# Kernel tuning notes

Hardware: AMD Instinct MI355X
Metric: run time of the kernel (lower is better)

Reference implementation:

```python
import jax, jax.numpy as jnp
import numpy as np

X_SCALE, X_ZP = 0.03, -66      # int8 quant params (qmin=-128, qmax=127)
Y_SCALE, Y_ZP = 0.025, 160     # uint8 quant params (qmin=0, qmax=255)
M = K = N = 4096


def setup_inputs() -> dict:
    key = jax.random.key(0)
    kx, ky = jax.random.split(key)
    # x holds int8-range values [-128, 127], y holds uint8-range values [0, 255]
    x = jax.random.randint(kx, (M, K), -128, 128, dtype=jnp.int32)
    y = jax.random.randint(ky, (K, N), 0, 256, dtype=jnp.int32)
    return {"x": x, "y": y}


def reference(x, y):
    # dequantize_per_tensor: (q - zero_point) * scale  (values already in [qmin, qmax])
    xf = (x.astype(jnp.float32) - X_ZP) * X_SCALE   # [M, K]
    yf = (y.astype(jnp.float32) - Y_ZP) * Y_SCALE   # [K, N]
    return jnp.matmul(xf, yf)                       # [M, N]
```

## Files before the change

### kernel.cpp

```cpp
#include <hip/hip_runtime.h>
#include <stdint.h>

#define Mdim 4096
#define Kdim 4096
#define Ndim 4096

typedef __attribute__((ext_vector_type(4))) int v4i;
typedef __attribute__((ext_vector_type(16))) int v16i;

__device__ __forceinline__ void gload_lds16(const void* g, void* l) {
  __builtin_amdgcn_global_load_lds(
      (__attribute__((address_space(1))) void*)(uintptr_t)g,
      (__attribute__((address_space(3))) void*)(uint32_t)(uintptr_t)l,
      16, 0, 0);
}

__global__ __launch_bounds__(256) void pack_fused_kernel(
    const int* __restrict__ x, const int* __restrict__ y,
    char* __restrict__ x8, char* __restrict__ yt, int* __restrict__ rsx,
    int* __restrict__ csy) {
  __shared__ int wt[64 * 17];
  const int t = threadIdx.x;
  if (blockIdx.x < Mdim) {
    const int row = blockIdx.x;
    const int4* src = (const int4*)(x + (size_t)row * Kdim);
    int4* dst = (int4*)(x8 + (size_t)row * Kdim);
    int sum = 0;
    int wd[4];
#pragma unroll
    for (int i = 0; i < 4; ++i) {
      int4 v = src[t * 4 + i];
      sum += v.x + v.y + v.z + v.w;
      wd[i] = (v.x & 0xff) | ((v.y & 0xff) << 8) | ((v.z & 0xff) << 16) |
              (v.w << 24);
    }
    dst[t] = make_int4(wd[0], wd[1], wd[2], wd[3]);
#pragma unroll
    for (int o = 32; o > 0; o >>= 1) sum += __shfl_down(sum, o, 64);
    if ((t & 63) == 0) wt[t >> 6] = sum;
    __syncthreads();
    if (t == 0) rsx[row] = wt[0] + wt[1] + wt[2] + wt[3];
  } else {
    const int bidx = blockIdx.x - Mdim;
    const int n0 = (bidx & 63) * 64;
    const int k0 = (bidx >> 6) * 64;
    const int c = t & 15;
    const int r0 = t >> 4;
#pragma unroll
    for (int s = 0; s < 4; ++s) {
      const int r = r0 + s * 16;
      int4 v = *(const int4*)(y + (size_t)(k0 + r) * Ndim + n0 + c * 4);
      v.x -= 128; v.y -= 128; v.z -= 128; v.w -= 128;
      wt[r * 17 + c] = (v.x & 0xff) | ((v.y & 0xff) << 8) |
                       ((v.z & 0xff) << 16) | (v.w << 24);
    }
    __syncthreads();
    const int n = t >> 2;
    const int kq = t & 3;
    const int colw = n >> 2;
    const int byi = (n & 3) * 8;
    int outw[4];
    int bsum = 0;
#pragma unroll
    for (int j = 0; j < 4; ++j) {
      int b[4];
#pragma unroll
      for (int jj = 0; jj < 4; ++jj) {
        const int word = wt[(kq * 16 + j * 4 + jj) * 17 + colw];
        b[jj] = (word >> byi) & 0xff;
        bsum += (int)(char)b[jj];
      }
      outw[j] = b[0] | (b[1] << 8) | (b[2] << 16) | (b[3] << 24);
    }
    *(int4*)(yt + (size_t)(n0 + n) * Kdim + k0 + kq * 16) =
        make_int4(outw[0], outw[1], outw[2], outw[3]);
    bsum += __shfl_xor(bsum, 1, 64);
    bsum += __shfl_xor(bsum, 2, 64);
    if (kq == 0) atomicAdd(csy + n0 + n, bsum);
  }
}

__global__ __launch_bounds__(512, 2) void gemm_i8_kernel(
    const char* __restrict__ A, const char* __restrict__ B,
    const int* __restrict__ rsx, const int* __restrict__ csy,
    float* __restrict__ out) {
  __shared__ __align__(16) char lds[3 * 32768];
  const int t = threadIdx.x;
  const int l = t & 63;
  const int w = t >> 6;
  const int warow = w >> 1;
  const int wbcol = w & 1;
  const int bm = blockIdx.y * 256;
  const int bn = blockIdx.x * 256;

  v16i acc[2][4];
#pragma unroll
  for (int i = 0; i < 2; ++i)
#pragma unroll
    for (int j = 0; j < 4; ++j)
#pragma unroll
      for (int q = 0; q < 16; ++q) acc[i][j][q] = 0;

  const int srow = t >> 2;
  const int cswz = ((t & 3) ^ ((t >> 3) & 3)) * 16;
  const char* gA = A + (size_t)(bm + srow) * Kdim + cswz;
  const char* gB = B + (size_t)(bn + srow) * Kdim + cswz;

#define STAGE(buf_off, koff)                                                  \
  do {                                                                        \
    _Pragma("unroll") for (int i = 0; i < 2; ++i)                             \
        gload_lds16(gA + (koff) + (size_t)i * 128 * Kdim,                     \
                    lds + (buf_off) + i * 8192 + t * 16);                     \
    _Pragma("unroll") for (int i = 0; i < 2; ++i)                             \
        gload_lds16(gB + (koff) + (size_t)i * 128 * Kdim,                     \
                    lds + (buf_off) + 16384 + i * 8192 + t * 16);             \
  } while (0)

#define STG(sbo, koff, idx)                                                   \
  gload_lds16(((idx) < 2 ? gA : gB) + (koff) + (size_t)((idx)&1) * 128 * Kdim,\
              lds + (sbo) + ((idx) < 2 ? 0 : 16384) + ((idx)&1) * 8192 +      \
                  t * 16)

  const int arow = warow * 64 + (l & 31);
  const int brow = wbcol * 128 + (l & 31);
  const int lhalf = l >> 5;
  const int lkey = (l >> 1) & 3;
  const int slot0 = ((0 + lhalf) ^ lkey) * 16;
  const int slot1 = ((2 + lhalf) ^ lkey) * 16;

#define MFMA(a, b, c) __builtin_amdgcn_mfma_i32_32x32x32_i8(a, b, c, 0, 0, 0)
#define SETP(n) __builtin_amdgcn_s_setprio(n)
#define FENCE() __builtin_amdgcn_sched_barrier(0)
#define BAR()                                                                 \
  do {                                                                        \
    asm volatile("" ::: "memory");                                            \
    __builtin_amdgcn_s_barrier();                                             \
    asm volatile("" ::: "memory");                                            \
  } while (0)
#define WAITV(n) asm volatile("s_waitcnt vmcnt(" #n ")" ::: "memory")

#define TILE(bo, sbo, skoff, dostage, TAILWAIT)                               \
  do {                                                                        \
    const char* As = lds + (bo);                                              \
    const char* Bs = lds + (bo) + 16384;                                      \
    v4i a0, a1, b0, b1;                                                       \
    a0 = *(const v4i*)(As + arow * 64 + slot0);                               \
    a1 = *(const v4i*)(As + (arow + 32) * 64 + slot0);                        \
    b0 = *(const v4i*)(Bs + brow * 64 + slot0);                               \
    b1 = *(const v4i*)(Bs + (brow + 32) * 64 + slot0);                        \
    if (dostage) STG(sbo, skoff, 0);                                          \
    BAR();                                                                    \
    FENCE();                                                                  \
    SETP(1);                                                                  \
    acc[0][0] = MFMA(a0, b0, acc[0][0]);                                      \
    acc[0][1] = MFMA(a0, b1, acc[0][1]);                                      \
    acc[1][0] = MFMA(a1, b0, acc[1][0]);                                      \
    acc[1][1] = MFMA(a1, b1, acc[1][1]);                                      \
    SETP(0);                                                                  \
    FENCE();                                                                  \
    BAR();                                                                    \
    {                                                                         \
      v4i b2 = *(const v4i*)(Bs + (brow + 64) * 64 + slot0);                  \
      v4i b3 = *(const v4i*)(Bs + (brow + 96) * 64 + slot0);                  \
      if (dostage) STG(sbo, skoff, 1);                                        \
      BAR();                                                                  \
      FENCE();                                                                \
      SETP(1);                                                                \
      acc[0][2] = MFMA(a0, b2, acc[0][2]);                                    \
      acc[0][3] = MFMA(a0, b3, acc[0][3]);                                    \
      acc[1][2] = MFMA(a1, b2, acc[1][2]);                                    \
      acc[1][3] = MFMA(a1, b3, acc[1][3]);                                    \
      SETP(0);                                                                \
      FENCE();                                                                \
      BAR();                                                                  \
    }                                                                         \
    a0 = *(const v4i*)(As + arow * 64 + slot1);                               \
    a1 = *(const v4i*)(As + (arow + 32) * 64 + slot1);                        \
    b0 = *(const v4i*)(Bs + brow * 64 + slot1);                               \
    b1 = *(const v4i*)(Bs + (brow + 32) * 64 + slot1);                        \
    if (dostage) STG(sbo, skoff, 2);                                          \
    BAR();                                                                    \
    FENCE();                                                                  \
    SETP(1);                                                                  \
    acc[0][0] = MFMA(a0, b0, acc[0][0]);                                      \
    acc[0][1] = MFMA(a0, b1, acc[0][1]);                                      \
    acc[1][0] = MFMA(a1, b0, acc[1][0]);                                      \
    acc[1][1] = MFMA(a1, b1, acc[1][1]);                                      \
    SETP(0);                                                                  \
    FENCE();                                                                  \
    BAR();                                                                    \
    {                                                                         \
      v4i b2 = *(const v4i*)(Bs + (brow + 64) * 64 + slot1);                  \
      v4i b3 = *(const v4i*)(Bs + (brow + 96) * 64 + slot1);                  \
      if (dostage) STG(sbo, skoff, 3);                                        \
      BAR();                                                                  \
      FENCE();                                                                \
      SETP(1);                                                                \
      acc[0][2] = MFMA(a0, b2, acc[0][2]);                                    \
      acc[0][3] = MFMA(a0, b3, acc[0][3]);                                    \
      acc[1][2] = MFMA(a1, b2, acc[1][2]);                                    \
      acc[1][3] = MFMA(a1, b3, acc[1][3]);                                    \
      SETP(0);                                                                \
      FENCE();                                                                \
      TAILWAIT;                                                               \
      BAR();                                                                  \
    }                                                                         \
  } while (0)

  STAGE(0, 0);
  STAGE(32768, 64);
  WAITV(4);
  BAR();

#pragma unroll 1
  for (int kt = 0; kt < 60; kt += 3) {
    TILE(0, 65536, (kt + 2) * 64, 1, WAITV(4));
    TILE(32768, 0, (kt + 3) * 64, 1, WAITV(4));
    TILE(65536, 32768, (kt + 4) * 64, 1, WAITV(4));
  }
  TILE(0, 65536, 62 * 64, 1, WAITV(4));
  TILE(32768, 0, 63 * 64, 1, WAITV(4));
  TILE(65536, 0, 0, 0, WAITV(0));
  TILE(0, 0, 0, 0, (void)0);

  const int col = l & 31;
#pragma unroll
  for (int i = 0; i < 2; ++i) {
    const int gm0 = bm + warow * 64 + i * 32;
#pragma unroll
    for (int j = 0; j < 4; ++j) {
      const int gn = bn + wbcol * 128 + j * 32 + col;
      const int cs = 66 * csy[gn] - 8650752;
#pragma unroll
      for (int r = 0; r < 16; ++r) {
        const int row = (r & 3) + 8 * (r >> 2) + 4 * lhalf;
        const int gm = gm0 + row;
        const int val = acc[i][j][r] - 32 * rsx[gm] + cs;
        out[(size_t)gm * Ndim + gn] = 7.5e-4f * (float)val;
      }
    }
  }
#undef STAGE
#undef STG
#undef TILE
#undef MFMA
#undef SETP
#undef FENCE
#undef BAR
#undef WAITV
}

extern "C" void kernel_launch(void* const* d_in, const int* in_sizes, int n_in,
                              void* d_out, int out_size, void* d_ws, size_t ws_size,
                              hipStream_t stream) {
  (void)in_sizes; (void)n_in; (void)out_size; (void)ws_size;
  const int* x = (const int*)d_in[0];
  const int* y = (const int*)d_in[1];
  float* out = (float*)d_out;
  char* ws = (char*)d_ws;
  char* x8 = ws;
  char* yt = ws + (size_t)Mdim * Kdim;
  int* rsx = (int*)(ws + (size_t)Mdim * Kdim + (size_t)Kdim * Ndim);
  int* csy = rsx + Mdim;

  hipMemsetAsync(csy, 0, Ndim * sizeof(int), stream);
  pack_fused_kernel<<<Mdim + (Ndim / 64) * (Kdim / 64), 256, 0, stream>>>(
      x, y, x8, yt, rsx, csy);
  gemm_i8_kernel<<<dim3(Ndim / 256, Mdim / 256), 512, 0, stream>>>(x8, yt, rsx,
                                                                   csy, out);
}
```

Baseline: 236.2 us.

## Restructure pack kernel: column-strip y transpose, drop memset and atomics

The y-transpose blocks now each own a 16-column strip across all of K, looping over 512-row chunks, so column sums are reduced in-block and written directly. This removes the hipMemsetAsync launch and the atomicAdd traffic. x-row packing is merged so that each 512-thread block handles two rows. The trade-off is fewer, longer-running y blocks (256), which could hurt load balance and latency hiding, and a narrow 16-column read per row that gives less coalesced global loads.

```diff
diff --git a/kernel.cpp b/kernel.cpp
--- a/kernel.cpp
+++ b/kernel.cpp
@@ -15,68 +15,76 @@
       16, 0, 0);
 }
 
-__global__ __launch_bounds__(256) void pack_fused_kernel(
+__global__ __launch_bounds__(512) void pack_fused_kernel(
     const int* __restrict__ x, const int* __restrict__ y,
     char* __restrict__ x8, char* __restrict__ yt, int* __restrict__ rsx,
     int* __restrict__ csy) {
-  __shared__ int wt[64 * 17];
+  __shared__ int shm[512 * 5];
   const int t = threadIdx.x;
-  if (blockIdx.x < Mdim) {
-    const int row = blockIdx.x;
+  if (blockIdx.x < 256) {
+    const int n0 = blockIdx.x * 16;
+    const int n = t >> 5;
+    const int kq = t & 31;
+    const int colw = n >> 2;
+    const int byi = (n & 3) * 8;
+    int bsum = 0;
+#pragma unroll 1
+    for (int c = 0; c < 8; ++c) {
+      const int k0 = c * 512;
+#pragma unroll
+      for (int p = 0; p < 4; ++p) {
+        const int r = (t >> 2) + p * 128;
+        int4 v = *(const int4*)(y + (size_t)(k0 + r) * Ndim + n0 + (t & 3) * 4);
+        int wd = (v.x & 0xff) | ((v.y & 0xff) << 8) | ((v.z & 0xff) << 16) |
+                 (v.w << 24);
+        shm[r * 5 + (t & 3)] = wd ^ 0x80808080;
+      }
+      __syncthreads();
+      int outw[4];
+#pragma unroll
+      for (int j = 0; j < 4; ++j) {
+        int b[4];
+#pragma unroll
+        for (int jj = 0; jj < 4; ++jj) {
+          const int word = shm[(kq * 16 + j * 4 + jj) * 5 + colw];
+          b[jj] = (word >> byi) & 0xff;
+          bsum += (int)(char)b[jj];
+        }
+        outw[j] = b[0] | (b[1] << 8) | (b[2] << 16) | (b[3] << 24);
+      }
+      *(int4*)(yt + (size_t)(n0 + n) * Kdim + k0 + kq * 16) =
+          make_int4(outw[0], outw[1], outw[2], outw[3]);
+      __syncthreads();
+    }
+    bsum += __shfl_xor(bsum, 1, 64);
+    bsum += __shfl_xor(bsum, 2, 64);
+    bsum += __shfl_xor(bsum, 4, 64);
+    bsum += __shfl_xor(bsum, 8, 64);
+    bsum += __shfl_xor(bsum, 16, 64);
+    if (kq == 0) csy[n0 + n] = bsum;
+  } else {
+    const int rowp = (int)(blockIdx.x - 256) * 2;
+    const int h = t >> 8;
+    const int tt = t & 255;
+    const int row = rowp + h;
     const int4* src = (const int4*)(x + (size_t)row * Kdim);
     int4* dst = (int4*)(x8 + (size_t)row * Kdim);
     int sum = 0;
     int wd[4];
 #pragma unroll
     for (int i = 0; i < 4; ++i) {
-      int4 v = src[t * 4 + i];
+      int4 v = src[tt * 4 + i];
       sum += v.x + v.y + v.z + v.w;
       wd[i] = (v.x & 0xff) | ((v.y & 0xff) << 8) | ((v.z & 0xff) << 16) |
               (v.w << 24);
     }
-    dst[t] = make_int4(wd[0], wd[1], wd[2], wd[3]);
+    dst[tt] = make_int4(wd[0], wd[1], wd[2], wd[3]);
 #pragma unroll
     for (int o = 32; o > 0; o >>= 1) sum += __shfl_down(sum, o, 64);
-    if ((t & 63) == 0) wt[t >> 6] = sum;
+    if ((t & 63) == 0) shm[t >> 6] = sum;
     __syncthreads();
-    if (t == 0) rsx[row] = wt[0] + wt[1] + wt[2] + wt[3];
-  } else {
-    const int bidx = blockIdx.x - Mdim;
-    const int n0 = (bidx & 63) * 64;
-    const int k0 = (bidx >> 6) * 64;
-    const int c = t & 15;
-    const int r0 = t >> 4;
-#pragma unroll
-    for (int s = 0; s < 4; ++s) {
-      const int r = r0 + s * 16;
-      int4 v = *(const int4*)(y + (size_t)(k0 + r) * Ndim + n0 + c * 4);
-      v.x -= 128; v.y -= 128; v.z -= 128; v.w -= 128;
-      wt[r * 17 + c] = (v.x & 0xff) | ((v.y & 0xff) << 8) |
-                       ((v.z & 0xff) << 16) | (v.w << 24);
-    }
-    __syncthreads();
-    const int n = t >> 2;
-    const int kq = t & 3;
-    const int colw = n >> 2;
-    const int byi = (n & 3) * 8;
-    int outw[4];
-    int bsum = 0;
-#pragma unroll
-    for (int j = 0; j < 4; ++j) {
-      int b[4];
-#pragma unroll
-      for (int jj = 0; jj < 4; ++jj) {
-        const int word = wt[(kq * 16 + j * 4 + jj) * 17 + colw];
-        b[jj] = (word >> byi) & 0xff;
-        bsum += (int)(char)b[jj];
-      }
-      outw[j] = b[0] | (b[1] << 8) | (b[2] << 16) | (b[3] << 24);
-    }
-    *(int4*)(yt + (size_t)(n0 + n) * Kdim + k0 + kq * 16) =
-        make_int4(outw[0], outw[1], outw[2], outw[3]);
-    bsum += __shfl_xor(bsum, 1, 64);
-    bsum += __shfl_xor(bsum, 2, 64);
-    if (kq == 0) atomicAdd(csy + n0 + n, bsum);
+    if (t == 0) rsx[rowp] = shm[0] + shm[1] + shm[2] + shm[3];
+    if (t == 256) rsx[rowp + 1] = shm[4] + shm[5] + shm[6] + shm[7];
   }
 }
 
@@ -263,9 +271,7 @@
   int* rsx = (int*)(ws + (size_t)Mdim * Kdim + (size_t)Kdim * Ndim);
   int* csy = rsx + Mdim;
 
-  hipMemsetAsync(csy, 0, Ndim * sizeof(int), stream);
-  pack_fused_kernel<<<Mdim + (Ndim / 64) * (Kdim / 64), 256, 0, stream>>>(
-      x, y, x8, yt, rsx, csy);
+  pack_fused_kernel<<<256 + Mdim / 2, 512, 0, stream>>>(x, y, x8, yt, rsx, csy);
   gemm_i8_kernel<<<dim3(Ndim / 256, Mdim / 256), 512, 0, stream>>>(x8, yt, rsx,
                                                                    csy, out);
 }
```

Result: slower. 244.8 us (+3.6%).
